# Optimization experiments

Hardware: AMD Instinct MI355X
Metric: run time of the kernel (lower is better)

## Reference

```python
import jax, jax.numpy as jnp
import numpy as np

BN_EPS = 1e-5
TAU = 1.0  # gumbel temperature

def setup_inputs() -> dict:
    key = jax.random.key(0)
    ks = jax.random.split(key, 6)
    B, O, F, H, HID = 32, 4096, 256, 8, 128
    x = jax.random.normal(ks[0], (B, O, F), dtype=jnp.float32)
    gumbel_noise = jax.random.gumbel(ks[1], (B, O, H), dtype=jnp.float32)
    W_in = jax.random.normal(ks[2], (F, HID), dtype=jnp.float32) * (1.0 / np.sqrt(F))
    b_in = jnp.zeros((HID,), jnp.float32)
    W_blk = jax.random.normal(ks[3], (HID, HID), dtype=jnp.float32) * (1.0 / np.sqrt(HID))
    b_blk = jnp.zeros((HID,), jnp.float32)
    bn_gamma = jnp.ones((HID,), jnp.float32)
    bn_beta = jnp.zeros((HID,), jnp.float32)
    W_fc = jax.random.normal(ks[4], (HID, H), dtype=jnp.float32) * (1.0 / np.sqrt(HID))
    b_fc = jnp.zeros((H,), jnp.float32)
    return {"x": x, "gumbel_noise": gumbel_noise, "W_in": W_in, "b_in": b_in,
            "W_blk": W_blk, "b_blk": b_blk, "bn_gamma": bn_gamma, "bn_beta": bn_beta,
            "W_fc": W_fc, "b_fc": b_fc}

def reference(x, gumbel_noise, W_in, b_in, W_blk, b_blk, bn_gamma, bn_beta, W_fc, b_fc):
    B, O, F = x.shape
    xf = x.reshape(B * O, F)
    # DynamicNetwork head: input linear + relu, one residual block (Linear+BN+ReLU), fc
    h = jax.nn.relu(xf @ W_in + b_in)  # (B*O, HID)
    z = h @ W_blk + b_blk
    mu = z.mean(axis=0)
    var = z.var(axis=0)  # biased var, matches BatchNorm training normalization
    z = (z - mu) * jax.lax.rsqrt(var + BN_EPS) * bn_gamma + bn_beta
    h = jax.nn.relu(z) + h  # residual
    logits = (h @ W_fc + b_fc).reshape(B, O, -1)  # (B, O, H)
    # mask out zero-norm observations
    mask = (jnp.linalg.norm(x, axis=2) != 0)[..., None].astype(x.dtype)  # (B, O, 1)
    logits = logits * mask
    # gumbel softmax over observation dim (soft)
    w = jax.nn.softmax((logits + gumbel_noise) / TAU, axis=1)  # (B, O, H)
    # weighted sum pooling: algebraically the repeat-multiply-sum in the original
    pooled = jnp.einsum('boh,bof->bhf', w, x)  # (B, H, F)
    return pooled.reshape(B, -1)  # (B, H*F)
```

## Files before the change

### kernel.cpp

```cpp
#include <hip/hip_runtime.h>
#include <hip/hip_bf16.h>
#include <math.h>

#define MB_ 131072
#define F_  256
#define HID_ 128
#define H_  8
#define O_  4096
#define B_  32

typedef __attribute__((ext_vector_type(8))) short short8;
typedef __attribute__((ext_vector_type(4))) float f32x4;

static __device__ __forceinline__ unsigned short f2bf(float f) {
    unsigned int u = __float_as_uint(f);
    unsigned int r = (u + 0x7fffu + ((u >> 16) & 1u)) >> 16;
    return (unsigned short)r;
}
static __device__ __forceinline__ float bf2f(unsigned short u) {
    return __uint_as_float(((unsigned int)u) << 16);
}
static __device__ __forceinline__ unsigned int pk2bf(float a, float b) {
    float2 f2; f2.x = a; f2.y = b;
    __hip_bfloat162 h = __float22bfloat162_rn(f2);
    union { __hip_bfloat162 h2; unsigned int u; } cv;
    cv.h2 = h;
    return cv.u;
}

__global__ __launch_bounds__(256) void k_prep(
    const float* __restrict__ W_in, const float* __restrict__ W_blk,
    unsigned short* __restrict__ WinT, unsigned short* __restrict__ WblkT)
{
    const int idx = blockIdx.x * 256 + threadIdx.x;
    if (idx < 32768) {
        const int n = idx >> 8, k = idx & 255;
        WinT[idx] = f2bf(W_in[(size_t)k * HID_ + n]);
    } else {
        const int i2 = idx - 32768;
        const int n = i2 >> 7, k = i2 & 127;
        WblkT[i2] = f2bf(W_blk[(size_t)k * HID_ + n]);
    }
}

__global__ __launch_bounds__(256, 4) void k_phaseA(
    const float* __restrict__ x, const unsigned short* __restrict__ WinT,
    const unsigned short* __restrict__ WblkT,
    const float* __restrict__ b_in, const float* __restrict__ b_blk,
    unsigned short* __restrict__ h_out, float* __restrict__ mask_out,
    float* __restrict__ sumP, float* __restrict__ sumsqP)
{
    __shared__ unsigned short hb_s[128 * 136];
    __shared__ float csum_s[128], csumsq_s[128];

    const int tid = threadIdx.x;
    const int R0 = blockIdx.x * 128;
    const int wave = tid >> 6;
    const int wrow = wave >> 1, wcol = wave & 1;
    const int lane = tid & 63;
    const int lm = lane & 15, quad = lane >> 4;

    if (tid < 128) { csum_s[tid] = 0.f; csumsq_s[tid] = 0.f; }

    f32x4 acc[4][4];
#pragma unroll
    for (int i = 0; i < 4; i++)
#pragma unroll
        for (int j = 0; j < 4; j++) acc[i][j] = (f32x4){0.f, 0.f, 0.f, 0.f};
    float ms[4] = {0.f, 0.f, 0.f, 0.f};

    const float* xb = x + (size_t)(R0 + wrow * 64 + lm) * F_;
    const unsigned short* wb = WinT + (size_t)(wcol * 64 + lm) * F_;

#pragma unroll 2
    for (int kt = 0; kt < 8; kt++) {
        const int kof = kt * 32 + quad * 8;
        short8 af[4], bfr[4];
#pragma unroll
        for (int mi = 0; mi < 4; mi++) {
            const float4 v0 = *(const float4*)(xb + (size_t)mi * 16 * F_ + kof);
            const float4 v1 = *(const float4*)(xb + (size_t)mi * 16 * F_ + kof + 4);
            ms[mi] += v0.x * v0.x + v0.y * v0.y + v0.z * v0.z + v0.w * v0.w
                    + v1.x * v1.x + v1.y * v1.y + v1.z * v1.z + v1.w * v1.w;
            union { short8 s8; unsigned int u[4]; } fr;
            fr.u[0] = pk2bf(v0.x, v0.y);
            fr.u[1] = pk2bf(v0.z, v0.w);
            fr.u[2] = pk2bf(v1.x, v1.y);
            fr.u[3] = pk2bf(v1.z, v1.w);
            af[mi] = fr.s8;
        }
#pragma unroll
        for (int ni = 0; ni < 4; ni++)
            bfr[ni] = *(const short8*)(wb + (size_t)ni * 16 * F_ + kof);
#pragma unroll
        for (int mi = 0; mi < 4; mi++)
#pragma unroll
            for (int ni = 0; ni < 4; ni++)
                acc[mi][ni] = __builtin_amdgcn_mfma_f32_16x16x32_bf16(af[mi], bfr[ni], acc[mi][ni], 0, 0, 0);
    }

#pragma unroll
    for (int mi = 0; mi < 4; mi++) {
        float s = ms[mi];
        s += __shfl_xor(s, 16);
        s += __shfl_xor(s, 32);
        if (wcol == 0 && quad == 0)
            mask_out[R0 + wrow * 64 + mi * 16 + lm] = (s != 0.f) ? 1.f : 0.f;
    }

    {
        float bcol[4];
#pragma unroll
        for (int ni = 0; ni < 4; ni++) bcol[ni] = b_in[wcol * 64 + ni * 16 + lm];
#pragma unroll
        for (int mi = 0; mi < 4; mi++)
#pragma unroll
            for (int r = 0; r < 4; r++) {
                const int row = wrow * 64 + mi * 16 + quad * 4 + r;
#pragma unroll
                for (int ni = 0; ni < 4; ni++) {
                    const int col = wcol * 64 + ni * 16 + lm;
                    hb_s[row * 136 + col] = f2bf(fmaxf(acc[mi][ni][r] + bcol[ni], 0.f));
                }
            }
    }
    __syncthreads();

    {
        const int row = tid >> 1, half = tid & 1;
#pragma unroll
        for (int c8 = 0; c8 < 8; c8++) {
            const short8 v = *(const short8*)(&hb_s[row * 136 + half * 64 + c8 * 8]);
            *(short8*)(h_out + (size_t)(R0 + row) * HID_ + half * 64 + c8 * 8) = v;
        }
    }

#pragma unroll
    for (int i = 0; i < 4; i++)
#pragma unroll
        for (int j = 0; j < 4; j++) acc[i][j] = (f32x4){0.f, 0.f, 0.f, 0.f};
    const unsigned short* wb2 = WblkT + (size_t)(wcol * 64 + lm) * HID_;
#pragma unroll
    for (int kt = 0; kt < 4; kt++) {
        const int kof = kt * 32 + quad * 8;
        short8 af[4], bfr[4];
#pragma unroll
        for (int mi = 0; mi < 4; mi++)
            af[mi] = *(const short8*)(&hb_s[(wrow * 64 + mi * 16 + lm) * 136 + kof]);
#pragma unroll
        for (int ni = 0; ni < 4; ni++)
            bfr[ni] = *(const short8*)(wb2 + (size_t)ni * 16 * HID_ + kof);
#pragma unroll
        for (int mi = 0; mi < 4; mi++)
#pragma unroll
            for (int ni = 0; ni < 4; ni++)
                acc[mi][ni] = __builtin_amdgcn_mfma_f32_16x16x32_bf16(af[mi], bfr[ni], acc[mi][ni], 0, 0, 0);
    }

    {
        float bcol[4];
#pragma unroll
        for (int ni = 0; ni < 4; ni++) bcol[ni] = b_blk[wcol * 64 + ni * 16 + lm];
        float s_c[4] = {0.f, 0.f, 0.f, 0.f}, ss_c[4] = {0.f, 0.f, 0.f, 0.f};
#pragma unroll
        for (int mi = 0; mi < 4; mi++)
#pragma unroll
            for (int r = 0; r < 4; r++)
#pragma unroll
                for (int ni = 0; ni < 4; ni++) {
                    const float zv = acc[mi][ni][r] + bcol[ni];
                    s_c[ni] += zv;
                    ss_c[ni] += zv * zv;
                }
#pragma unroll
        for (int ni = 0; ni < 4; ni++) {
            float s = s_c[ni], ss = ss_c[ni];
            s  += __shfl_xor(s, 16);  s  += __shfl_xor(s, 32);
            ss += __shfl_xor(ss, 16); ss += __shfl_xor(ss, 32);
            if (quad == 0) {
                atomicAdd(&csum_s[wcol * 64 + ni * 16 + lm], s);
                atomicAdd(&csumsq_s[wcol * 64 + ni * 16 + lm], ss);
            }
        }
    }
    __syncthreads();
    if (tid < 128) {
        sumP[(size_t)blockIdx.x * 128 + tid] = csum_s[tid];
        sumsqP[(size_t)blockIdx.x * 128 + tid] = csumsq_s[tid];
    }
}

__global__ __launch_bounds__(256) void k_bnfin(
    const float* __restrict__ sumP, const float* __restrict__ sumsqP,
    const float* __restrict__ gamma, const float* __restrict__ beta,
    float* __restrict__ scale, float* __restrict__ shift)
{
    const int c = blockIdx.x;
    const int tid = threadIdx.x;
    float s = 0.f, ss = 0.f;
    for (int i = tid; i < 1024; i += 256) {
        s  += sumP[(size_t)i * 128 + c];
        ss += sumsqP[(size_t)i * 128 + c];
    }
#pragma unroll
    for (int off = 32; off; off >>= 1) {
        s  += __shfl_xor(s, off, 64);
        ss += __shfl_xor(ss, off, 64);
    }
    __shared__ float rs[4], rss[4];
    const int wid = tid >> 6, lane = tid & 63;
    if (lane == 0) { rs[wid] = s; rss[wid] = ss; }
    __syncthreads();
    if (tid == 0) {
        const float S  = rs[0] + rs[1] + rs[2] + rs[3];
        const float SS = rss[0] + rss[1] + rss[2] + rss[3];
        const float inv_m = 1.0f / (float)MB_;
        const float mu = S * inv_m;
        const float var = SS * inv_m - mu * mu;
        const float sc = gamma[c] * rsqrtf(var + 1e-5f);
        scale[c] = sc;
        shift[c] = beta[c] - mu * sc;
    }
}

__global__ __launch_bounds__(256, 4) void k_phaseC(
    const unsigned short* __restrict__ h_in, const unsigned short* __restrict__ WblkT,
    const float* __restrict__ b_blk,
    const float* __restrict__ scale, const float* __restrict__ shift,
    const float* __restrict__ W_fc, const float* __restrict__ b_fc,
    const float* __restrict__ mask, const float* __restrict__ gumbel,
    float* __restrict__ t_bho)
{
    __shared__ unsigned short hb_s[128 * 136];
    __shared__ float wfc_s[128 * 8];
    __shared__ float sc_s[128], sh_s[128];

    const int tid = threadIdx.x;
    const int R0 = blockIdx.x * 128;
    const int wave = tid >> 6;
    const int wrow = wave >> 1, wcol = wave & 1;
    const int lane = tid & 63;
    const int lm = lane & 15, quad = lane >> 4;

    for (int i = tid; i < 1024; i += 256) wfc_s[i] = W_fc[i];
    if (tid < 128) { sc_s[tid] = scale[tid]; sh_s[tid] = shift[tid]; }
    {
        const int row = tid >> 1, half = tid & 1;
#pragma unroll
        for (int c8 = 0; c8 < 8; c8++) {
            const short8 v = *(const short8*)(h_in + (size_t)(R0 + row) * HID_ + half * 64 + c8 * 8);
            *(short8*)(&hb_s[row * 136 + half * 64 + c8 * 8]) = v;
        }
    }
    __syncthreads();

    f32x4 acc[4][4];
#pragma unroll
    for (int i = 0; i < 4; i++)
#pragma unroll
        for (int j = 0; j < 4; j++) acc[i][j] = (f32x4){0.f, 0.f, 0.f, 0.f};
    const unsigned short* wb2 = WblkT + (size_t)(wcol * 64 + lm) * HID_;
#pragma unroll
    for (int kt = 0; kt < 4; kt++) {
        const int kof = kt * 32 + quad * 8;
        short8 af[4], bfr[4];
#pragma unroll
        for (int mi = 0; mi < 4; mi++)
            af[mi] = *(const short8*)(&hb_s[(wrow * 64 + mi * 16 + lm) * 136 + kof]);
#pragma unroll
        for (int ni = 0; ni < 4; ni++)
            bfr[ni] = *(const short8*)(wb2 + (size_t)ni * 16 * HID_ + kof);
#pragma unroll
        for (int mi = 0; mi < 4; mi++)
#pragma unroll
            for (int ni = 0; ni < 4; ni++)
                acc[mi][ni] = __builtin_amdgcn_mfma_f32_16x16x32_bf16(af[mi], bfr[ni], acc[mi][ni], 0, 0, 0);
    }

    {
        float bcol[4];
#pragma unroll
        for (int ni = 0; ni < 4; ni++) bcol[ni] = b_blk[wcol * 64 + ni * 16 + lm];
#pragma unroll
        for (int mi = 0; mi < 4; mi++)
#pragma unroll
            for (int r = 0; r < 4; r++) {
                const int row = wrow * 64 + mi * 16 + quad * 4 + r;
#pragma unroll
                for (int ni = 0; ni < 4; ni++) {
                    const int col = wcol * 64 + ni * 16 + lm;
                    const float zv = acc[mi][ni][r] + bcol[ni];
                    const float hv = bf2f(hb_s[row * 136 + col]);
                    const float hb = fmaxf(zv * sc_s[col] + sh_s[col], 0.f) + hv;
                    hb_s[row * 136 + col] = f2bf(hb);
                }
            }
    }
    __syncthreads();

    if (tid < 128) {
        const int row = tid;
        const int grow = R0 + row;
        const int b = grow >> 12, o = grow & 4095;
        float a8[8];
#pragma unroll
        for (int j = 0; j < 8; j++) a8[j] = 0.f;
#pragma unroll 4
        for (int k8 = 0; k8 < 16; k8++) {
            const short8 hv8 = *(const short8*)(&hb_s[row * 136 + k8 * 8]);
#pragma unroll
            for (int e = 0; e < 8; e++) {
                const float hv = bf2f((unsigned short)hv8[e]);
                const int k = k8 * 8 + e;
#pragma unroll
                for (int j = 0; j < 8; j++) a8[j] += hv * wfc_s[k * 8 + j];
            }
        }
        const float mk = mask[grow];
        const float* gp = gumbel + (size_t)grow * 8;
#pragma unroll
        for (int j = 0; j < 8; j++) {
            const float t = (a8[j] + b_fc[j]) * mk + gp[j];
            t_bho[((size_t)(b * 8 + j)) * O_ + o] = t;
        }
    }
}

__global__ __launch_bounds__(256) void k_softmax(
    const float* __restrict__ t_in, float* __restrict__ w_out)
{
    const int bh = blockIdx.x;
    const int tid = threadIdx.x;
    const float* tp = t_in + (size_t)bh * O_;
    float4 v[4];
    float mx = -3.4e38f;
#pragma unroll
    for (int it = 0; it < 4; it++) {
        v[it] = *(const float4*)(tp + it * 1024 + tid * 4);
        mx = fmaxf(mx, fmaxf(fmaxf(v[it].x, v[it].y), fmaxf(v[it].z, v[it].w)));
    }
#pragma unroll
    for (int off = 32; off; off >>= 1) mx = fmaxf(mx, __shfl_xor(mx, off, 64));
    __shared__ float rm[4], rsum[4];
    const int wid = tid >> 6, lane = tid & 63;
    if (lane == 0) rm[wid] = mx;
    __syncthreads();
    mx = fmaxf(fmaxf(rm[0], rm[1]), fmaxf(rm[2], rm[3]));
    float sum = 0.f;
#pragma unroll
    for (int it = 0; it < 4; it++) {
        v[it].x = __expf(v[it].x - mx); v[it].y = __expf(v[it].y - mx);
        v[it].z = __expf(v[it].z - mx); v[it].w = __expf(v[it].w - mx);
        sum += v[it].x + v[it].y + v[it].z + v[it].w;
    }
#pragma unroll
    for (int off = 32; off; off >>= 1) sum += __shfl_xor(sum, off, 64);
    if (lane == 0) rsum[wid] = sum;
    __syncthreads();
    sum = rsum[0] + rsum[1] + rsum[2] + rsum[3];
    const float inv = 1.f / sum;
    float* wp = w_out + (size_t)bh * O_;
#pragma unroll
    for (int it = 0; it < 4; it++) {
        float4 o;
        o.x = v[it].x * inv; o.y = v[it].y * inv; o.z = v[it].z * inv; o.w = v[it].w * inv;
        *(float4*)(wp + it * 1024 + tid * 4) = o;
    }
}

__global__ __launch_bounds__(256) void k_pool(
    const float* __restrict__ x, const float* __restrict__ w_in,
    float* __restrict__ pp)
{
    __shared__ float ws_s[8][128];
    const int tid = threadIdx.x;
    const int oc = blockIdx.x;
    const int b = blockIdx.y;
    const int wave = tid >> 6, lane = tid & 63;
    const int f = wave * 64 + lane;
    for (int i = tid; i < 1024; i += 256) {
        const int hh = i >> 7, oi = i & 127;
        ws_s[hh][oi] = w_in[((size_t)(b * 8 + hh)) * O_ + oc * 128 + oi];
    }
    __syncthreads();
    float acc[8];
#pragma unroll
    for (int hh = 0; hh < 8; hh++) acc[hh] = 0.f;
    const float* xp = x + ((size_t)(b * O_ + oc * 128)) * F_ + f;
#pragma unroll 1
    for (int oi = 0; oi < 128; oi += 4) {
        float xv[4];
#pragma unroll
        for (int u = 0; u < 4; u++) xv[u] = xp[(size_t)(oi + u) * F_];
#pragma unroll
        for (int u = 0; u < 4; u++)
#pragma unroll
            for (int hh = 0; hh < 8; hh++) acc[hh] += ws_s[hh][oi + u] * xv[u];
    }
    float* outp = pp + ((size_t)(oc * 32 + b)) * 2048;
#pragma unroll
    for (int hh = 0; hh < 8; hh++) outp[hh * 256 + f] = acc[hh];
}

__global__ __launch_bounds__(256) void k_reduce_pool(
    const float* __restrict__ pp, float* __restrict__ out)
{
    const size_t i = (size_t)blockIdx.x * 256 + threadIdx.x;
    float s = 0.f;
#pragma unroll
    for (int oc = 0; oc < 32; oc++) s += pp[(size_t)oc * 65536 + i];
    out[i] = s;
}

extern "C" void kernel_launch(void* const* d_in, const int* in_sizes, int n_in,
                              void* d_out, int out_size, void* d_ws, size_t ws_size,
                              hipStream_t stream)
{
    const float* x      = (const float*)d_in[0];
    const float* gumbel = (const float*)d_in[1];
    const float* W_in   = (const float*)d_in[2];
    const float* b_in   = (const float*)d_in[3];
    const float* W_blk  = (const float*)d_in[4];
    const float* b_blk  = (const float*)d_in[5];
    const float* gamma  = (const float*)d_in[6];
    const float* beta   = (const float*)d_in[7];
    const float* W_fc   = (const float*)d_in[8];
    const float* b_fc   = (const float*)d_in[9];
    float* out = (float*)d_out;
    char* ws = (char*)d_ws;

    unsigned short* h_bf  = (unsigned short*)(ws + 0);
    float* mask   = (float*)(ws + 33554432);
    float* sumP   = (float*)(ws + 34078720);
    float* sumsqP = (float*)(ws + 34603008);
    float* scale  = (float*)(ws + 35127296);
    float* shift  = (float*)(ws + 35127808);
    float* t_buf  = (float*)(ws + 35128320);
    float* w_buf  = (float*)(ws + 39322624);
    float* pp     = (float*)(ws + 43516928);
    unsigned short* WinT  = (unsigned short*)(ws + 51905536);
    unsigned short* WblkT = (unsigned short*)(ws + 51971072);

    k_prep<<<192, 256, 0, stream>>>(W_in, W_blk, WinT, WblkT);
    k_phaseA<<<1024, 256, 0, stream>>>(x, WinT, WblkT, b_in, b_blk, h_bf, mask, sumP, sumsqP);
    k_bnfin<<<128, 256, 0, stream>>>(sumP, sumsqP, gamma, beta, scale, shift);
    k_phaseC<<<1024, 256, 0, stream>>>(h_bf, WblkT, b_blk, scale, shift, W_fc, b_fc, mask, gumbel, t_buf);
    k_softmax<<<256, 256, 0, stream>>>(t_buf, w_buf);
    k_pool<<<dim3(32, 32), 256, 0, stream>>>(x, w_buf, pp);
    k_reduce_pool<<<256, 256, 0, stream>>>(pp, out);
}
```

Before: 313.0 us.

## Stage x tiles through double-buffered LDS and pre-swizzle weights into MFMA fragment layout

Phase A now loads x cooperatively with coalesced float4 reads, converts it to bf16, and stages it in a double-buffered LDS tile. The next k-slice is prefetched while the MFMAs run, replacing per-wave strided global loads where each wave re-read x rows that other waves also needed. The weights are rearranged in the prep kernel into a fragment-contiguous layout so each B-fragment load is a contiguous 16-byte read. Phase C's final projection now uses all 256 threads, with two threads per row combined by a shuffle. In exchange, Phase A uses more LDS and a barrier per k-step, and its occupancy hint drops from 4 to 3.

Measured after the change: 331.4 us. +5.9%, slower.

```diff
diff --git a/kernel.cpp b/kernel.cpp
--- a/kernel.cpp
+++ b/kernel.cpp
@@ -30,27 +30,28 @@
 
 __global__ __launch_bounds__(256) void k_prep(
     const float* __restrict__ W_in, const float* __restrict__ W_blk,
-    unsigned short* __restrict__ WinT, unsigned short* __restrict__ WblkT)
+    unsigned short* __restrict__ Win_f, unsigned short* __restrict__ Wblk_f)
 {
     const int idx = blockIdx.x * 256 + threadIdx.x;
     if (idx < 32768) {
-        const int n = idx >> 8, k = idx & 255;
-        WinT[idx] = f2bf(W_in[(size_t)k * HID_ + n]);
-    } else {
+        const int j = idx & 7, n = (idx >> 3) & 127, c = idx >> 10;
+        Win_f[idx] = f2bf(W_in[(size_t)(c * 8 + j) * HID_ + n]);
+    } else if (idx < 49152) {
         const int i2 = idx - 32768;
-        const int n = i2 >> 7, k = i2 & 127;
-        WblkT[i2] = f2bf(W_blk[(size_t)k * HID_ + n]);
-    }
-}
-
-__global__ __launch_bounds__(256, 4) void k_phaseA(
-    const float* __restrict__ x, const unsigned short* __restrict__ WinT,
-    const unsigned short* __restrict__ WblkT,
+        const int j = i2 & 7, n = (i2 >> 3) & 127, c = i2 >> 10;
+        Wblk_f[i2] = f2bf(W_blk[(size_t)(c * 8 + j) * HID_ + n]);
+    }
+}
+
+__global__ __launch_bounds__(256, 3) void k_phaseA(
+    const float* __restrict__ x, const unsigned short* __restrict__ Win_f,
+    const unsigned short* __restrict__ Wblk_f,
     const float* __restrict__ b_in, const float* __restrict__ b_blk,
     unsigned short* __restrict__ h_out, float* __restrict__ mask_out,
     float* __restrict__ sumP, float* __restrict__ sumsqP)
 {
-    __shared__ unsigned short hb_s[128 * 136];
+    __shared__ __align__(16) unsigned short a_s[2][4 * 132 * 8];
+    __shared__ __align__(16) unsigned short hb_s[128 * 136];
     __shared__ float csum_s[128], csumsq_s[128];
 
     const int tid = threadIdx.x;
@@ -59,6 +60,9 @@
     const int wrow = wave >> 1, wcol = wave & 1;
     const int lane = tid & 63;
     const int lm = lane & 15, quad = lane >> 4;
+    const int srow = tid >> 3;
+    const int sk = tid & 7;
+    const int sq = sk >> 1, sh = sk & 1;
 
     if (tid < 128) { csum_s[tid] = 0.f; csumsq_s[tid] = 0.f; }
 
@@ -69,43 +73,57 @@
         for (int j = 0; j < 4; j++) acc[i][j] = (f32x4){0.f, 0.f, 0.f, 0.f};
     float ms[4] = {0.f, 0.f, 0.f, 0.f};
 
-    const float* xb = x + (size_t)(R0 + wrow * 64 + lm) * F_;
-    const unsigned short* wb = WinT + (size_t)(wcol * 64 + lm) * F_;
-
-#pragma unroll 2
+    const float* xrow = x + (size_t)(R0 + srow) * F_ + sk * 4;
+
+#pragma unroll
+    for (int p = 0; p < 4; p++) {
+        const float4 v = *(const float4*)(xrow + (size_t)(32 * p) * F_);
+        ms[p] += v.x * v.x + v.y * v.y + v.z * v.z + v.w * v.w;
+        uint2 w; w.x = pk2bf(v.x, v.y); w.y = pk2bf(v.z, v.w);
+        *(uint2*)(&a_s[0][(sq * 132 + srow + 32 * p) * 8 + sh * 4]) = w;
+    }
+    __syncthreads();
+
     for (int kt = 0; kt < 8; kt++) {
-        const int kof = kt * 32 + quad * 8;
-        short8 af[4], bfr[4];
-#pragma unroll
-        for (int mi = 0; mi < 4; mi++) {
-            const float4 v0 = *(const float4*)(xb + (size_t)mi * 16 * F_ + kof);
-            const float4 v1 = *(const float4*)(xb + (size_t)mi * 16 * F_ + kof + 4);
-            ms[mi] += v0.x * v0.x + v0.y * v0.y + v0.z * v0.z + v0.w * v0.w
-                    + v1.x * v1.x + v1.y * v1.y + v1.z * v1.z + v1.w * v1.w;
-            union { short8 s8; unsigned int u[4]; } fr;
-            fr.u[0] = pk2bf(v0.x, v0.y);
-            fr.u[1] = pk2bf(v0.z, v0.w);
-            fr.u[2] = pk2bf(v1.x, v1.y);
-            fr.u[3] = pk2bf(v1.z, v1.w);
-            af[mi] = fr.s8;
-        }
+        const int cur = kt & 1;
+        float4 nv[4];
+        if (kt < 7) {
+#pragma unroll
+            for (int p = 0; p < 4; p++)
+                nv[p] = *(const float4*)(xrow + (kt + 1) * 32 + (size_t)(32 * p) * F_);
+        }
+        short8 bfr[4], af[4];
+        const unsigned short* wf = Win_f + ((size_t)(kt * 4 + quad) * 128 + wcol * 64 + lm) * 8;
 #pragma unroll
         for (int ni = 0; ni < 4; ni++)
-            bfr[ni] = *(const short8*)(wb + (size_t)ni * 16 * F_ + kof);
+            bfr[ni] = *(const short8*)(wf + ni * 16 * 8);
+#pragma unroll
+        for (int mi = 0; mi < 4; mi++)
+            af[mi] = *(const short8*)(&a_s[cur][(quad * 132 + wrow * 64 + mi * 16 + lm) * 8]);
 #pragma unroll
         for (int mi = 0; mi < 4; mi++)
 #pragma unroll
             for (int ni = 0; ni < 4; ni++)
                 acc[mi][ni] = __builtin_amdgcn_mfma_f32_16x16x32_bf16(af[mi], bfr[ni], acc[mi][ni], 0, 0, 0);
-    }
-
-#pragma unroll
-    for (int mi = 0; mi < 4; mi++) {
-        float s = ms[mi];
-        s += __shfl_xor(s, 16);
-        s += __shfl_xor(s, 32);
-        if (wcol == 0 && quad == 0)
-            mask_out[R0 + wrow * 64 + mi * 16 + lm] = (s != 0.f) ? 1.f : 0.f;
+        if (kt < 7) {
+#pragma unroll
+            for (int p = 0; p < 4; p++) {
+                ms[p] += nv[p].x * nv[p].x + nv[p].y * nv[p].y
+                       + nv[p].z * nv[p].z + nv[p].w * nv[p].w;
+                uint2 w; w.x = pk2bf(nv[p].x, nv[p].y); w.y = pk2bf(nv[p].z, nv[p].w);
+                *(uint2*)(&a_s[1 - cur][(sq * 132 + srow + 32 * p) * 8 + sh * 4]) = w;
+            }
+        }
+        __syncthreads();
+    }
+
+#pragma unroll
+    for (int p = 0; p < 4; p++) {
+        float s = ms[p];
+        s += __shfl_down(s, 4, 8);
+        s += __shfl_down(s, 2, 8);
+        s += __shfl_down(s, 1, 8);
+        if (sk == 0) mask_out[R0 + srow + 32 * p] = (s != 0.f) ? 1.f : 0.f;
     }
 
     {
@@ -139,17 +157,16 @@
     for (int i = 0; i < 4; i++)
 #pragma unroll
         for (int j = 0; j < 4; j++) acc[i][j] = (f32x4){0.f, 0.f, 0.f, 0.f};
-    const unsigned short* wb2 = WblkT + (size_t)(wcol * 64 + lm) * HID_;
 #pragma unroll
     for (int kt = 0; kt < 4; kt++) {
-        const int kof = kt * 32 + quad * 8;
         short8 af[4], bfr[4];
-#pragma unroll
-        for (int mi = 0; mi < 4; mi++)
-            af[mi] = *(const short8*)(&hb_s[(wrow * 64 + mi * 16 + lm) * 136 + kof]);
+        const unsigned short* wf2 = Wblk_f + ((size_t)(kt * 4 + quad) * 128 + wcol * 64 + lm) * 8;
 #pragma unroll
         for (int ni = 0; ni < 4; ni++)
-            bfr[ni] = *(const short8*)(wb2 + (size_t)ni * 16 * HID_ + kof);
+            bfr[ni] = *(const short8*)(wf2 + ni * 16 * 8);
+#pragma unroll
+        for (int mi = 0; mi < 4; mi++)
+            af[mi] = *(const short8*)(&hb_s[(wrow * 64 + mi * 16 + lm) * 136 + kt * 32 + quad * 8]);
 #pragma unroll
         for (int mi = 0; mi < 4; mi++)
 #pragma unroll
@@ -224,14 +241,14 @@
 }
 
 __global__ __launch_bounds__(256, 4) void k_phaseC(
-    const unsigned short* __restrict__ h_in, const unsigned short* __restrict__ WblkT,
+    const unsigned short* __restrict__ h_in, const unsigned short* __restrict__ Wblk_f,
     const float* __restrict__ b_blk,
     const float* __restrict__ scale, const float* __restrict__ shift,
     const float* __restrict__ W_fc, const float* __restrict__ b_fc,
     const float* __restrict__ mask, const float* __restrict__ gumbel,
     float* __restrict__ t_bho)
 {
-    __shared__ unsigned short hb_s[128 * 136];
+    __shared__ __align__(16) unsigned short hb_s[128 * 136];
     __shared__ float wfc_s[128 * 8];
     __shared__ float sc_s[128], sh_s[128];
 
@@ -259,17 +276,16 @@
     for (int i = 0; i < 4; i++)
 #pragma unroll
         for (int j = 0; j < 4; j++) acc[i][j] = (f32x4){0.f, 0.f, 0.f, 0.f};
-    const unsigned short* wb2 = WblkT + (size_t)(wcol * 64 + lm) * HID_;
 #pragma unroll
     for (int kt = 0; kt < 4; kt++) {
-        const int kof = kt * 32 + quad * 8;
         short8 af[4], bfr[4];
-#pragma unroll
-        for (int mi = 0; mi < 4; mi++)
-            af[mi] = *(const short8*)(&hb_s[(wrow * 64 + mi * 16 + lm) * 136 + kof]);
+        const unsigned short* wf2 = Wblk_f + ((size_t)(kt * 4 + quad) * 128 + wcol * 64 + lm) * 8;
 #pragma unroll
         for (int ni = 0; ni < 4; ni++)
-            bfr[ni] = *(const short8*)(wb2 + (size_t)ni * 16 * HID_ + kof);
+            bfr[ni] = *(const short8*)(wf2 + ni * 16 * 8);
+#pragma unroll
+        for (int mi = 0; mi < 4; mi++)
+            af[mi] = *(const short8*)(&hb_s[(wrow * 64 + mi * 16 + lm) * 136 + kt * 32 + quad * 8]);
 #pragma unroll
         for (int mi = 0; mi < 4; mi++)
 #pragma unroll
@@ -298,29 +314,31 @@
     }
     __syncthreads();
 
-    if (tid < 128) {
-        const int row = tid;
+    {
+        const int row = tid >> 1, half = tid & 1;
         const int grow = R0 + row;
-        const int b = grow >> 12, o = grow & 4095;
         float a8[8];
 #pragma unroll
         for (int j = 0; j < 8; j++) a8[j] = 0.f;
-#pragma unroll 4
-        for (int k8 = 0; k8 < 16; k8++) {
-            const short8 hv8 = *(const short8*)(&hb_s[row * 136 + k8 * 8]);
+#pragma unroll 2
+        for (int k8 = 0; k8 < 8; k8++) {
+            const short8 hv8 = *(const short8*)(&hb_s[row * 136 + half * 64 + k8 * 8]);
 #pragma unroll
             for (int e = 0; e < 8; e++) {
                 const float hv = bf2f((unsigned short)hv8[e]);
-                const int k = k8 * 8 + e;
+                const int k = half * 64 + k8 * 8 + e;
 #pragma unroll
                 for (int j = 0; j < 8; j++) a8[j] += hv * wfc_s[k * 8 + j];
             }
         }
+#pragma unroll
+        for (int j = 0; j < 8; j++) a8[j] += __shfl_xor(a8[j], 1);
         const float mk = mask[grow];
-        const float* gp = gumbel + (size_t)grow * 8;
-#pragma unroll
-        for (int j = 0; j < 8; j++) {
-            const float t = (a8[j] + b_fc[j]) * mk + gp[j];
+        const int b = grow >> 12, o = grow & 4095;
+#pragma unroll
+        for (int jj = 0; jj < 4; jj++) {
+            const int j = half * 4 + jj;
+            const float t = (a8[j] + b_fc[j]) * mk + gumbel[(size_t)grow * 8 + j];
             t_bho[((size_t)(b * 8 + j)) * O_ + o] = t;
         }
     }
@@ -438,13 +456,13 @@
     float* t_buf  = (float*)(ws + 35128320);
     float* w_buf  = (float*)(ws + 39322624);
     float* pp     = (float*)(ws + 43516928);
-    unsigned short* WinT  = (unsigned short*)(ws + 51905536);
-    unsigned short* WblkT = (unsigned short*)(ws + 51971072);
-
-    k_prep<<<192, 256, 0, stream>>>(W_in, W_blk, WinT, WblkT);
-    k_phaseA<<<1024, 256, 0, stream>>>(x, WinT, WblkT, b_in, b_blk, h_bf, mask, sumP, sumsqP);
+    unsigned short* Win_f  = (unsigned short*)(ws + 51905536);
+    unsigned short* Wblk_f = (unsigned short*)(ws + 51971072);
+
+    k_prep<<<192, 256, 0, stream>>>(W_in, W_blk, Win_f, Wblk_f);
+    k_phaseA<<<1024, 256, 0, stream>>>(x, Win_f, Wblk_f, b_in, b_blk, h_bf, mask, sumP, sumsqP);
     k_bnfin<<<128, 256, 0, stream>>>(sumP, sumsqP, gamma, beta, scale, shift);
-    k_phaseC<<<1024, 256, 0, stream>>>(h_bf, WblkT, b_blk, scale, shift, W_fc, b_fc, mask, gumbel, t_buf);
+    k_phaseC<<<1024, 256, 0, stream>>>(h_bf, Wblk_f, b_blk, scale, shift, W_fc, b_fc, mask, gumbel, t_buf);
     k_softmax<<<256, 256, 0, stream>>>(t_buf, w_buf);
     k_pool<<<dim3(32, 32), 256, 0, stream>>>(x, w_buf, pp);
     k_reduce_pool<<<256, 256, 0, stream>>>(pp, out);
```
